# Performance work log

Measured on AMD Instinct MI355X. Metric: run time of the kernel, lower is better.

## Reference

```python
import jax, jax.numpy as jnp
import numpy as np

B, C, H, W = 16, 64, 256, 256
STRIDE = 2
IN_KS = 3
OUT_KS = 3  # must be odd
HP, WP = H // STRIDE, W // STRIDE


def setup_inputs() -> dict:
    key = jax.random.key(0)
    k1, k2, k3 = jax.random.split(key, 3)
    f = jax.random.normal(k1, (B, C, HP, WP), dtype=jnp.float32)
    # Provenance: for pooled cell (i, j), the argmax location within the
    # IN_KS x IN_KS window anchored at (i*STRIDE, j*STRIDE), as a flat h*w index.
    dy = jax.random.randint(k2, (B, C, HP, WP), 0, IN_KS)
    dx = jax.random.randint(k3, (B, C, HP, WP), 0, IN_KS)
    rows = jnp.clip(jnp.arange(HP)[None, None, :, None] * STRIDE + dy, 0, H - 1)
    cols = jnp.clip(jnp.arange(WP)[None, None, None, :] * STRIDE + dx, 0, W - 1)
    provenance = (rows * W + cols).astype(jnp.int32)
    return {"f": f, "provenance": provenance, "h": H, "w": W}


def reference(f, provenance, h, w):
    b, c, hp, wp = f.shape
    # --- unpool: scatter pooled values to provenance locations in an h*w canvas ---
    vals = f.reshape(b * c, hp * wp)
    idx = provenance.reshape(b * c, hp * wp)
    scatter = lambda i, v: jnp.zeros((h * w,), f.dtype).at[i].set(v)
    up = jax.vmap(scatter)(idx, vals).reshape(b, c, h, w)
    # --- dilation: OUT_KS x OUT_KS windowed max, stride 1, 'same' padding ---
    p = (OUT_KS - 1) // 2
    out = jax.lax.reduce_window(
        up, -jnp.inf, jax.lax.max,
        window_dimensions=(1, 1, OUT_KS, OUT_KS),
        window_strides=(1, 1, 1, 1),
        padding=[(0, 0), (0, 0), (p, p), (p, p)],
    )
    return out
```

## Files before the change

### kernel.cpp

```cpp
#include <hip/hip_runtime.h>
#include <math.h>

#define BATCH 16
#define CHAN  64
#define Hh    256
#define Ww    256
#define HP    128
#define WP    128
#define TH    64
#define TW    64
#define CH    66
#define CW    66
#define CS    68

typedef unsigned int u32;
typedef float vfloat4 __attribute__((ext_vector_type(4)));

__global__ __launch_bounds__(256, 8) void unpool_dilate_kernel(
    const float* __restrict__ f, const int* __restrict__ prov,
    float* __restrict__ out)
{
    __shared__ __align__(16) u32 s[CH * CS];

    const int tid = threadIdx.x;
    const int bc  = blockIdx.y;
    const int ty  = blockIdx.x >> 2;
    const int tx  = blockIdx.x & 3;
    const int y0  = ty * TH;
    const int x0  = tx * TW;

    const int pi_min = (ty == 0) ? 0 : (ty * 32 - 1);
    const int pj_min = (tx == 0) ? 0 : (tx * 32 - 1);
    const int pi_max = min(HP - 1, ty * 32 + 32);
    const int pj_max = min(WP - 1, tx * 32 + 32);
    const size_t in_base = (size_t)bc * (HP * WP);

    u32   m_key[5];
    float m_f[5];
    int   m_p[5];
    #pragma unroll
    for (int it = 0; it < 5; ++it) {
        m_key[it] = 0u;
        const int k = tid + it * 256;
        if (k < 34 * 34) {
            const int ki = k / 34;
            const int kj = k - ki * 34;
            const bool valid = (pi_min + ki <= pi_max) & (pj_min + kj <= pj_max);
            const int pi = min(pi_min + ki, pi_max);
            const int pj = min(pj_min + kj, pj_max);
            const int q  = pi * WP + pj;
            m_key[it] = valid ? (u32)(q + 1) : 0u;
            m_p[it]   = prov[in_base + q];
            m_f[it]   = f[in_base + q];
        }
    }

    {
        const u32 NI = 0xFF800000u;
        uint4* p4 = (uint4*)s;
        #pragma unroll
        for (int it = 0; it < 5; ++it) {
            const int idx = tid + it * 256;
            if (idx < (CH * CS) / 4) {
                const int row = idx / 17;
                const int c4w = (idx - row * 17) * 4;
                const bool rinf = ((ty == 0) & (row == 0)) |
                                  ((ty == 3) & (row == CH - 1));
                uint4 v;
                v.x = (rinf | ((tx == 0) & (c4w == 0)))  ? NI : 0u;
                v.y = (rinf | ((tx == 3) & (c4w == 64))) ? NI : 0u;
                v.z = rinf ? NI : 0u;
                v.w = rinf ? NI : 0u;
                p4[idx] = v;
            }
        }
    }
    __syncthreads();

    int m_li[5];
    #pragma unroll
    for (int it = 0; it < 5; ++it) {
        m_li[it] = -1;
        if (m_key[it]) {
            const int p  = m_p[it];
            const int lr = (p >> 8) - y0 + 1;
            const int lc = (p & 255) - x0 + 1;
            if ((unsigned)lr < CH && (unsigned)lc < CW) {
                const int li = lr * CS + lc;
                m_li[it] = li;
                atomicMax(&s[li], m_key[it]);
            }
        }
    }
    __syncthreads();

    #pragma unroll
    for (int it = 0; it < 5; ++it) {
        if (m_li[it] >= 0 && s[m_li[it]] == m_key[it])
            s[m_li[it]] = __float_as_uint(m_f[it]);
    }
    __syncthreads();

    const float* sf = (const float*)s;
    const int tr = tid >> 4;
    const int tc = tid & 15;
    const int r0 = 4 * tr;
    const int c0 = 4 * tc;

    float h0[4], h1[4];
    const size_t obase = (size_t)bc * (Hh * Ww) + (size_t)(y0 + r0) * Ww + (x0 + c0);

    #pragma unroll
    for (int r = 0; r < 6; ++r) {
        const float* row = sf + (r0 + r) * CS + c0;
        const float4 a = *(const float4*)row;
        const float2 b = *(const float2*)(row + 4);
        float h[4];
        h[0] = fmaxf(fmaxf(a.x, a.y), a.z);
        h[1] = fmaxf(fmaxf(a.y, a.z), a.w);
        h[2] = fmaxf(fmaxf(a.z, a.w), b.x);
        h[3] = fmaxf(fmaxf(a.w, b.x), b.y);
        if (r >= 2) {
            vfloat4 res;
            res.x = fmaxf(fmaxf(h0[0], h1[0]), h[0]);
            res.y = fmaxf(fmaxf(h0[1], h1[1]), h[1]);
            res.z = fmaxf(fmaxf(h0[2], h1[2]), h[2]);
            res.w = fmaxf(fmaxf(h0[3], h1[3]), h[3]);
            __builtin_nontemporal_store(res, (vfloat4*)(out + obase + (size_t)(r - 2) * Ww));
        }
        #pragma unroll
        for (int j = 0; j < 4; ++j) { h0[j] = h1[j]; h1[j] = h[j]; }
    }
}

extern "C" void kernel_launch(void* const* d_in, const int* in_sizes, int n_in,
                              void* d_out, int out_size, void* d_ws, size_t ws_size,
                              hipStream_t stream) {
    const float* f    = (const float*)d_in[0];
    const int*   prov = (const int*)d_in[1];
    float* out = (float*)d_out;

    dim3 grid((Hh / TH) * (Ww / TW), BATCH * CHAN);
    unpool_dilate_kernel<<<grid, 256, 0, stream>>>(f, prov, out);
}
```

Measured before the change: 364.6 us.

## Replace atomic scatter unpool with gather over 2x2 source cells per canvas unit

Instead of zero-filling shared memory and scattering pooled values with atomicMax plus a resolution pass, each thread owns a 2x2 canvas unit. It reads the four pooled cells whose 3x3 windows can reach that unit and selects matching provenance values, writing the unit directly. This removes two barriers, the atomics and the separate init pass, at the cost of redundant global loads, since each pooled cell is read by up to four threads and mostly hits in cache. Clamping at the borders and the last-writer priority order must reproduce the reference's scatter semantics for colliding indices.

```diff
diff --git a/kernel.cpp b/kernel.cpp
--- a/kernel.cpp
+++ b/kernel.cpp
@@ -12,6 +12,7 @@
 #define CH    66
 #define CW    66
 #define CS    68
+#define NUNIT 33
 
 typedef unsigned int u32;
 typedef float vfloat4 __attribute__((ext_vector_type(4)));
@@ -20,7 +21,7 @@
     const float* __restrict__ f, const int* __restrict__ prov,
     float* __restrict__ out)
 {
-    __shared__ __align__(16) u32 s[CH * CS];
+    __shared__ __align__(16) float s[CH * CS];
 
     const int tid = threadIdx.x;
     const int bc  = blockIdx.y;
@@ -29,79 +30,72 @@
     const int y0  = ty * TH;
     const int x0  = tx * TW;
 
-    const int pi_min = (ty == 0) ? 0 : (ty * 32 - 1);
-    const int pj_min = (tx == 0) ? 0 : (tx * 32 - 1);
-    const int pi_max = min(HP - 1, ty * 32 + 32);
-    const int pj_max = min(WP - 1, tx * 32 + 32);
     const size_t in_base = (size_t)bc * (HP * WP);
+    const int a0 = (y0 >> 1) - 1;
+    const int b0 = (x0 >> 1) - 1;
+    const float NINF = __int_as_float(0xFF800000u);
 
-    u32   m_key[5];
-    float m_f[5];
-    int   m_p[5];
     #pragma unroll
     for (int it = 0; it < 5; ++it) {
-        m_key[it] = 0u;
         const int k = tid + it * 256;
-        if (k < 34 * 34) {
-            const int ki = k / 34;
-            const int kj = k - ki * 34;
-            const bool valid = (pi_min + ki <= pi_max) & (pj_min + kj <= pj_max);
-            const int pi = min(pi_min + ki, pi_max);
-            const int pj = min(pj_min + kj, pj_max);
-            const int q  = pi * WP + pj;
-            m_key[it] = valid ? (u32)(q + 1) : 0u;
-            m_p[it]   = prov[in_base + q];
-            m_f[it]   = f[in_base + q];
-        }
-    }
+        if (k < NUNIT * NUNIT) {
+            const int ua = k / NUNIT;
+            const int ub = k - ua * NUNIT;
+            const int a  = a0 + ua;
+            const int b  = b0 + ub;
 
-    {
-        const u32 NI = 0xFF800000u;
-        uint4* p4 = (uint4*)s;
-        #pragma unroll
-        for (int it = 0; it < 5; ++it) {
-            const int idx = tid + it * 256;
-            if (idx < (CH * CS) / 4) {
-                const int row = idx / 17;
-                const int c4w = (idx - row * 17) * 4;
-                const bool rinf = ((ty == 0) & (row == 0)) |
-                                  ((ty == 3) & (row == CH - 1));
-                uint4 v;
-                v.x = (rinf | ((tx == 0) & (c4w == 0)))  ? NI : 0u;
-                v.y = (rinf | ((tx == 3) & (c4w == 64))) ? NI : 0u;
-                v.z = rinf ? NI : 0u;
-                v.w = rinf ? NI : 0u;
-                p4[idx] = v;
-            }
+            const int r0 = min(max(a, 0), HP - 2);
+            const int c0 = min(max(b, 0), WP - 2);
+            const size_t cell = in_base + (size_t)(r0 * WP + c0);
+            const int*   pp = prov + cell;
+            const float* pf = f    + cell;
+            const int   p00 = pp[0], p01 = pp[1], p10 = pp[WP], p11 = pp[WP + 1];
+            const float f00 = pf[0], f01 = pf[1], f10 = pf[WP], f11 = pf[WP + 1];
+
+            const int u0g = 2 * a + 1;
+            const int v0g = 2 * b + 1;
+            const int k00 = u0g * Ww + v0g;
+            const int k01 = k00 + 1;
+            const int k10 = k00 + Ww;
+            const int k11 = k10 + 1;
+
+            const bool inu0 = (u32)u0g       < (u32)Hh;
+            const bool inu1 = (u32)(u0g + 1) < (u32)Hh;
+            const bool inv0 = (u32)v0g       < (u32)Ww;
+            const bool inv1 = (u32)(v0g + 1) < (u32)Ww;
+            float v00 = (inu0 & inv0) ? 0.0f : NINF;
+            float v01 = (inu0 & inv1) ? 0.0f : NINF;
+            float v10 = (inu1 & inv0) ? 0.0f : NINF;
+            float v11 = (inu1 & inv1) ? 0.0f : NINF;
+
+            v00 = (p00 == k00) ? f00 : v00;
+            v01 = (p00 == k01) ? f00 : v01;
+            v10 = (p00 == k10) ? f00 : v10;
+            v11 = (p00 == k11) ? f00 : v11;
+
+            v00 = (p01 == k00) ? f01 : v00;
+            v01 = (p01 == k01) ? f01 : v01;
+            v10 = (p01 == k10) ? f01 : v10;
+            v11 = (p01 == k11) ? f01 : v11;
+
+            v00 = (p10 == k00) ? f10 : v00;
+            v01 = (p10 == k01) ? f10 : v01;
+            v10 = (p10 == k10) ? f10 : v10;
+            v11 = (p10 == k11) ? f10 : v11;
+
+            v00 = (p11 == k00) ? f11 : v00;
+            v01 = (p11 == k01) ? f11 : v01;
+            v10 = (p11 == k10) ? f11 : v10;
+            v11 = (p11 == k11) ? f11 : v11;
+
+            const int cbase = (2 * ua) * CS + 2 * ub;
+            *(float2*)&s[cbase]      = make_float2(v00, v01);
+            *(float2*)&s[cbase + CS] = make_float2(v10, v11);
         }
     }
     __syncthreads();
 
-    int m_li[5];
-    #pragma unroll
-    for (int it = 0; it < 5; ++it) {
-        m_li[it] = -1;
-        if (m_key[it]) {
-            const int p  = m_p[it];
-            const int lr = (p >> 8) - y0 + 1;
-            const int lc = (p & 255) - x0 + 1;
-            if ((unsigned)lr < CH && (unsigned)lc < CW) {
-                const int li = lr * CS + lc;
-                m_li[it] = li;
-                atomicMax(&s[li], m_key[it]);
-            }
-        }
-    }
-    __syncthreads();
-
-    #pragma unroll
-    for (int it = 0; it < 5; ++it) {
-        if (m_li[it] >= 0 && s[m_li[it]] == m_key[it])
-            s[m_li[it]] = __float_as_uint(m_f[it]);
-    }
-    __syncthreads();
-
-    const float* sf = (const float*)s;
+    const float* sf = s;
     const int tr = tid >> 4;
     const int tc = tid & 15;
     const int r0 = 4 * tr;
```

Result: slower. 379.6 us (+4.1%).
